# Kernel tuning notes

Hardware: AMD Instinct MI355X
Metric: run time of the kernel (lower is better)

## Reference

```python
import jax, jax.numpy as jnp
import numpy as np

B, TV, TE = 128, 32, 64
VOCAB, EMB, H, REPR, NET, MAXLEN = 1024, 256, 512, 128, 8, 32


def setup_inputs() -> dict:
    key = jax.random.key(0)
    ks = jax.random.split(key, 26)
    g = lambda i, shape: jax.random.normal(ks[i], shape, dtype=jnp.float32) * 0.05
    return dict(
        input_vertex=jax.random.randint(ks[0], (B, TV), 0, VOCAB),
        input_edge=jax.random.randint(ks[1], (B, TE, 3), 0, NET),
        vertex_emb=g(2, (VOCAB, EMB)),
        v_Wi=g(3, (3 * H, EMB)), v_Wh=g(4, (3 * H, H)), v_bi=g(5, (3 * H,)), v_bh=g(6, (3 * H,)),
        vout_W=g(7, (VOCAB, H)), vout_b=g(8, (VOCAB,)),
        vrep_W=g(9, (REPR, H)), vrep_b=g(10, (REPR,)),
        edge_emb=g(11, (MAXLEN, EMB)),
        e_Wi=g(12, (3 * H, 2 * EMB)), e_Wh=g(13, (3 * H, H)), e_bi=g(14, (3 * H,)), e_bh=g(15, (3 * H,)),
        erep_W=g(16, (REPR, H)), erep_b=g(17, (REPR,)),
        etype_W=g(18, (NET, REPR)), etype_b=g(19, (NET,)),
        src_w=g(20, (REPR,)), src_b=g(21, ()),
        dst_w=g(22, (REPR,)), dst_b=g(23, ()),
    )


def _gru_scan(X, Wi, Wh, bi, bh):
    # X: [T, B, D] -> hidden states [T, B, H]; torch GRUCell gate order r,z,n
    gi = jnp.einsum('tbd,gd->tbg', X, Wi) + bi  # precompute input projections
    h0 = jnp.zeros((X.shape[1], Wh.shape[1]), X.dtype)

    def step(h, gi_t):
        gh = h @ Wh.T + bh
        ir, iz, inn = jnp.split(gi_t, 3, axis=-1)
        hr, hz, hn = jnp.split(gh, 3, axis=-1)
        r = jax.nn.sigmoid(ir + hr)
        z = jax.nn.sigmoid(iz + hz)
        n = jnp.tanh(inn + r * hn)
        h_new = (1.0 - z) * n + z * h
        return h_new, h_new

    _, hs = jax.lax.scan(step, h0, gi)
    return hs


def reference(input_vertex, input_edge, vertex_emb, v_Wi, v_Wh, v_bi, v_bh,
              vout_W, vout_b, vrep_W, vrep_b, edge_emb, e_Wi, e_Wh, e_bi, e_bh,
              erep_W, erep_b, etype_W, etype_b, src_w, src_b, dst_w, dst_b):
    # ---- vertex RNN ----
    Ve = vertex_emb[input_vertex].transpose(1, 0, 2)          # [Tv, B, emb]
    hv = _gru_scan(Ve, v_Wi, v_Wh, v_bi, v_bh)                # [Tv, B, H]
    O_vertex = jnp.einsum('tbh,vh->bvt', hv, vout_W) + vout_b[None, :, None]  # [B, vocab, Tv]
    vrep = jnp.einsum('tbh,rh->tbr', hv, vrep_W) + vrep_b     # [Tv, B, repr]

    # ---- edge RNN ----
    E = jnp.concatenate([edge_emb[input_edge[:, :, 0]],
                         edge_emb[input_edge[:, :, 1]]], axis=2)  # [B, Te, 2*emb]
    he = _gru_scan(E.transpose(1, 0, 2), e_Wi, e_Wh, e_bi, e_bh)  # [Te, B, H]
    e = jnp.einsum('tbh,rh->tbr', he, erep_W) + erep_b            # [Te, B, repr]
    O_edge_type = jnp.einsum('ebr,kr->bke', e, etype_W) + etype_b[None, :, None]  # [B, n_et, Te]

    # ---- edge-vertex additive attention: tanh(e + v) ----
    u = jnp.tanh(e[:, None] + vrep[None])                     # [Te, Tv, B, repr]
    osrc = jnp.einsum('evbr,r->bve', u, src_w) + src_b        # [B, Tv, Te]
    odst = jnp.einsum('evbr,r->bve', u, dst_w) + dst_b        # [B, Tv, Te]
    O_edge = jnp.stack([osrc, odst], axis=2)                  # [B, Tv, 2, Te]

    return O_vertex, O_edge, O_edge_type
```

## Files before the change

### kernel.cpp

```cpp
#include <hip/hip_runtime.h>
#include <hip/hip_bf16.h>


typedef __bf16 bf16_t;
typedef bf16_t bf16x8 __attribute__((ext_vector_type(8)));
typedef bf16_t bf16x4 __attribute__((ext_vector_type(4)));
typedef float  f32x4  __attribute__((ext_vector_type(4)));

#define OFF_GIV  0ull
#define OFF_GIE  6291456ull
#define OFF_HV   18874368ull
#define OFF_HE   20971520ull
#define OFF_VREP 25165824ull
#define OFF_EREP 25690112ull
#define OFF_HBUF 26738688ull
#define FLAG_BYTE_OFF 54001664ull
#define OFF_CVT  27002880ull
#define CVT_VEMB  0ull
#define CVT_EEMB  262144ull
#define CVT_VWI   270336ull
#define CVT_EWI   663552ull
#define CVT_VWH   1449984ull
#define CVT_EWH   2236416ull
#define CVT_VOUT  3022848ull
#define CVT_VREPW 3547136ull
#define CVT_EREPW 3612672ull

#define OUT_OV 0ull
#define OUT_OE 4194304ull
#define OUT_OT 4718592ull

__device__ __forceinline__ float fsigmoid(float x) {
    float e = __builtin_amdgcn_exp2f(-x * 1.4426950408889634f);
    return __builtin_amdgcn_rcpf(1.0f + e);
}
__device__ __forceinline__ float ftanh(float x) {
    x = fminf(x, 15.0f);
    float e = __builtin_amdgcn_exp2f(x * 2.8853900817779268f);
    return (e - 1.0f) * __builtin_amdgcn_rcpf(e + 1.0f);
}

__global__ __launch_bounds__(256) void prep_kernel(
    const float* __restrict__ vemb, const float* __restrict__ eemb,
    const float* __restrict__ vwi,  const float* __restrict__ ewi,
    const float* __restrict__ vwh,  const float* __restrict__ ewh,
    const float* __restrict__ voutw, const float* __restrict__ vrepw,
    const float* __restrict__ erepw, bf16_t* __restrict__ cvt)
{
    int blk = blockIdx.x;
    const float* src; bf16_t* dst; int lb;
    if (blk < 256)       { src = vemb;  dst = cvt + CVT_VEMB;  lb = blk; }
    else if (blk < 264)  { src = eemb;  dst = cvt + CVT_EEMB;  lb = blk - 256; }
    else if (blk < 648)  { src = vwi;   dst = cvt + CVT_VWI;   lb = blk - 264; }
    else if (blk < 1416) { src = ewi;   dst = cvt + CVT_EWI;   lb = blk - 648; }
    else if (blk < 2184) { src = vwh;   dst = cvt + CVT_VWH;   lb = blk - 1416; }
    else if (blk < 2952) { src = ewh;   dst = cvt + CVT_EWH;   lb = blk - 2184; }
    else if (blk < 3464) { src = voutw; dst = cvt + CVT_VOUT;  lb = blk - 2952; }
    else if (blk < 3528) { src = vrepw; dst = cvt + CVT_VREPW; lb = blk - 3464; }
    else                 { src = erepw; dst = cvt + CVT_EREPW; lb = blk - 3528; }
    int idx = lb * 1024 + threadIdx.x * 4;
    float4 v = *(const float4*)(src + idx);
    bf16x4 o;
    o[0] = (bf16_t)v.x; o[1] = (bf16_t)v.y; o[2] = (bf16_t)v.z; o[3] = (bf16_t)v.w;
    *(bf16x4*)(dst + idx) = o;
}

template<int GATHER, int K>
__device__ __forceinline__ void produce_gi(
    const bf16_t* __restrict__ W, const float* __restrict__ bias,
    bf16_t* __restrict__ C, const int* __restrict__ gidx,
    const bf16_t* __restrict__ emb, int bx, int nbase)
{
    constexpr int K32 = K / 32;
    const int tid = threadIdx.x, lane = tid & 63, wv = tid >> 6;
    const int r16 = lane & 15, quad = lane >> 4, koff = quad * 8;
    const int mbase = bx * 512 + wv * 64;

    const bf16_t* ap0[4];
    const bf16_t* ap1[4];
#pragma unroll
    for (int i = 0; i < 4; ++i) {
        int row = mbase + i * 16 + r16;
        int b = row & 127, t = row >> 7;
        if (GATHER == 1) {
            ap0[i] = emb + (size_t)gidx[b * 32 + t] * 256 + koff;
            ap1[i] = ap0[i];
        } else {
            int c = (b * 64 + t) * 3;
            ap0[i] = emb + (size_t)gidx[c] * 256 + koff;
            ap1[i] = emb + (size_t)gidx[c + 1] * 256 + koff;
        }
    }
    const bf16_t* bp[4];
#pragma unroll
    for (int j = 0; j < 4; ++j)
        bp[j] = W + (size_t)(nbase + j * 16 + r16) * K + koff;

    f32x4 acc[4][4];
#pragma unroll
    for (int i = 0; i < 4; ++i)
#pragma unroll
        for (int j = 0; j < 4; ++j) acc[i][j] = (f32x4){0.f, 0.f, 0.f, 0.f};

    for (int kc = 0; kc < K32; ++kc) {
        bf16x8 a[4], b[4];
#pragma unroll
        for (int i = 0; i < 4; ++i) {
            const bf16_t* p;
            if (GATHER == 2) p = (kc < 8) ? (ap0[i] + kc * 32) : (ap1[i] + (kc - 8) * 32);
            else             p = ap0[i] + kc * 32;
            a[i] = *(const bf16x8*)p;
        }
#pragma unroll
        for (int j = 0; j < 4; ++j) b[j] = *(const bf16x8*)(bp[j] + kc * 32);
#pragma unroll
        for (int i = 0; i < 4; ++i)
#pragma unroll
            for (int j = 0; j < 4; ++j)
                acc[i][j] = __builtin_amdgcn_mfma_f32_16x16x32_bf16(a[i], b[j], acc[i][j], 0, 0, 0);
    }

#pragma unroll
    for (int j = 0; j < 4; ++j) {
        int col = nbase + j * 16 + r16;
        float bf = bias[col];
#pragma unroll
        for (int i = 0; i < 4; ++i) {
#pragma unroll
            for (int q = 0; q < 4; ++q) {
                int row = mbase + i * 16 + quad * 4 + q;
                C[(size_t)row * 1536 + col] = (bf16_t)(acc[i][j][q] + bf);
            }
        }
    }
}

__global__ __launch_bounds__(512) void produce_kernel(
    bf16_t* __restrict__ giV, bf16_t* __restrict__ giE,
    const int* __restrict__ ivtx, const int* __restrict__ iedg,
    const bf16_t* __restrict__ vemb, const bf16_t* __restrict__ eemb,
    const bf16_t* __restrict__ vwi, const bf16_t* __restrict__ ewi,
    const float* __restrict__ vbi, const float* __restrict__ ebi)
{
    int bid = blockIdx.x;
    if (bid < 192) {
        produce_gi<1, 256>(vwi, vbi, giV, ivtx, vemb, bid & 7, (bid >> 3) * 64);
    } else {
        int g3 = bid - 192;
        produce_gi<2, 512>(ewi, ebi, giE, iedg, eemb, g3 & 15, (g3 >> 4) * 64);
    }
}

__global__ __launch_bounds__(512)
__attribute__((amdgpu_waves_per_eu(2, 2)))
void gru_scan(
    const bf16_t* __restrict__ giV, const bf16_t* __restrict__ giE,
    const bf16_t* __restrict__ WhV, const bf16_t* __restrict__ WhE,
    const float* __restrict__ bhV, const float* __restrict__ bhE,
    bf16_t* __restrict__ hV, bf16_t* __restrict__ hE,
    bf16_t* __restrict__ hbuf, int* __restrict__ flags)
{
    __shared__ __align__(16) bf16_t hbf[2][16][520];
    __shared__ __align__(16) f32x4 red[4][3][64];
    const int bid = blockIdx.x;

    const int role = bid >> 6;
    const int lb   = bid & 63;
    const int g    = lb & 7;
    const int s    = lb >> 3;
    const bf16_t* gi = role ? giE : giV;
    const bf16_t* Wh = role ? WhE : WhV;
    const float*  bh = role ? bhE : bhV;
    bf16_t* hout = role ? hE : hV;
    const int T = role ? 64 : 32;
    const int slot = role * 8 + g;
    bf16_t* buf0 = hbuf + (size_t)slot * 2 * 8192;
    int* fl = flags + slot * 8;
    const int bb = g * 16;

    const int tid = threadIdx.x, lane = tid & 63, wv = tid >> 6;
    const int team = wv >> 1, half = wv & 1;
    const int r16 = lane & 15, quad = lane >> 4, koff = quad * 8;
    const int j = s * 64 + team * 16 + r16;
    const int kbase = half * 256;

    bf16x8 wfrag[3][8];
#pragma unroll
    for (int gate = 0; gate < 3; ++gate) {
        const bf16_t* wrow = Wh + ((size_t)(gate * 512 + j)) * 512 + kbase + koff;
#pragma unroll
        for (int kc = 0; kc < 8; ++kc)
            wfrag[gate][kc] = *(const bf16x8*)(wrow + kc * 32);
    }
    const float bhr = bh[j], bhz = bh[512 + j], bhn = bh[1024 + j];
    float hq[4] = {0.f, 0.f, 0.f, 0.f};

    for (int i = tid; i < 16 * 512; i += 512)
        hbf[0][i >> 9][i & 511] = (bf16_t)0.f;

    for (int t = 0; t < T; ++t) {
        if (t > 0) {
            if (wv == 1) {
                while (!__all((int)(__hip_atomic_load(&fl[lane & 7], __ATOMIC_RELAXED,
                                                      __HIP_MEMORY_SCOPE_AGENT) >= t))) { }
            }
            __syncthreads();
            asm volatile("" ::: "memory");
            unsigned long long* src = (unsigned long long*)(buf0 + (size_t)(t & 1) * 8192);
#pragma unroll
            for (int k = 0; k < 4; ++k) {
                int u = tid + k * 512;
                unsigned long long vv = __hip_atomic_load(src + u, __ATOMIC_RELAXED,
                                                          __HIP_MEMORY_SCOPE_AGENT);
                *(unsigned long long*)&hbf[t & 1][u >> 7][(u & 127) * 4] = vv;
            }
        }
        __syncthreads();

        float gv[3][4];
        if (half == 0) {
#pragma unroll
            for (int gg = 0; gg < 3; ++gg)
#pragma unroll
                for (int q = 0; q < 4; ++q)
                    gv[gg][q] = (float)gi[((size_t)(t * 128 + bb + quad * 4 + q)) * 1536
                                          + gg * 512 + j];
        }

        const bf16_t (*cur)[520] = hbf[t & 1];
        f32x4 ar = {0.f,0.f,0.f,0.f}, az = {0.f,0.f,0.f,0.f}, an = {0.f,0.f,0.f,0.f};
#pragma unroll
        for (int kc = 0; kc < 8; ++kc) {
            bf16x8 a = *(const bf16x8*)&cur[r16][kbase + kc * 32 + koff];
            ar = __builtin_amdgcn_mfma_f32_16x16x32_bf16(a, wfrag[0][kc], ar, 0, 0, 0);
            az = __builtin_amdgcn_mfma_f32_16x16x32_bf16(a, wfrag[1][kc], az, 0, 0, 0);
            an = __builtin_amdgcn_mfma_f32_16x16x32_bf16(a, wfrag[2][kc], an, 0, 0, 0);
        }

        if (half == 1) {
            red[team][0][lane] = ar;
            red[team][1][lane] = az;
            red[team][2][lane] = an;
        }
        __syncthreads();

        bf16_t hb4[4];
        if (half == 0) {
            ar += red[team][0][lane];
            az += red[team][1][lane];
            an += red[team][2][lane];
#pragma unroll
            for (int q = 0; q < 4; ++q) {
                float r = fsigmoid(gv[0][q] + ar[q] + bhr);
                float z = fsigmoid(gv[1][q] + az[q] + bhz);
                float n = ftanh(gv[2][q] + r * (an[q] + bhn));
                float hnew = (1.0f - z) * n + z * hq[q];
                hq[q] = hnew;
                hb4[q] = (bf16_t)hnew;
            }
            if (t + 1 < T) {
                bf16_t* dstg = buf0 + (size_t)((t + 1) & 1) * 8192;
#pragma unroll
                for (int q = 0; q < 4; ++q)
                    __hip_atomic_store((unsigned short*)(dstg + (quad * 4 + q) * 512 + j),
                                       __builtin_bit_cast(unsigned short, hb4[q]),
                                       __ATOMIC_RELAXED, __HIP_MEMORY_SCOPE_AGENT);
            }
        }

        if (t + 1 < T) {
            __builtin_amdgcn_s_waitcnt(0);
            __syncthreads();
            if (tid == 0)
                __hip_atomic_store(&fl[s], t + 1,
                                   __ATOMIC_RELAXED, __HIP_MEMORY_SCOPE_AGENT);
        } else {
            __syncthreads();
        }
        if (half == 0) {
#pragma unroll
            for (int q = 0; q < 4; ++q)
                hout[((size_t)((bb + quad * 4 + q) * T + t)) * 512 + j] = hb4[q];
        }
    }
}

template<int OUTMODE, int K>
__device__ __forceinline__ void consume_gemm(
    const bf16_t* __restrict__ A, const bf16_t* __restrict__ W,
    const float* __restrict__ bias, void* __restrict__ Cv,
    int N, int bx, int nbase)
{
    constexpr int K32 = K / 32;
    const int tid = threadIdx.x, lane = tid & 63, wv = tid >> 6;
    const int r16 = lane & 15, quad = lane >> 4, koff = quad * 8;
    const int mbase = bx * 512 + wv * 64;

    const bf16_t* ap[4];
#pragma unroll
    for (int i = 0; i < 4; ++i)
        ap[i] = A + (size_t)(mbase + i * 16 + r16) * K + koff;
    const bf16_t* bp[4];
#pragma unroll
    for (int j = 0; j < 4; ++j)
        bp[j] = W + (size_t)(nbase + j * 16 + r16) * K + koff;

    f32x4 acc[4][4];
#pragma unroll
    for (int i = 0; i < 4; ++i)
#pragma unroll
        for (int j = 0; j < 4; ++j) acc[i][j] = (f32x4){0.f, 0.f, 0.f, 0.f};

    for (int kc = 0; kc < K32; ++kc) {
        bf16x8 a[4], b[4];
#pragma unroll
        for (int i = 0; i < 4; ++i) a[i] = *(const bf16x8*)(ap[i] + kc * 32);
#pragma unroll
        for (int j = 0; j < 4; ++j) b[j] = *(const bf16x8*)(bp[j] + kc * 32);
#pragma unroll
        for (int i = 0; i < 4; ++i)
#pragma unroll
            for (int j = 0; j < 4; ++j)
                acc[i][j] = __builtin_amdgcn_mfma_f32_16x16x32_bf16(a[i], b[j], acc[i][j], 0, 0, 0);
    }

#pragma unroll
    for (int j = 0; j < 4; ++j) {
        int col = nbase + j * 16 + r16;
        float bf = bias[col];
#pragma unroll
        for (int i = 0; i < 4; ++i) {
            int rowq = mbase + i * 16 + quad * 4;
            if (OUTMODE == 1) {
                int b = rowq >> 5, t0 = rowq & 31;
                float4 v4;
                v4.x = acc[i][j][0] + bf; v4.y = acc[i][j][1] + bf;
                v4.z = acc[i][j][2] + bf; v4.w = acc[i][j][3] + bf;
                *(float4*)((float*)Cv + ((size_t)(b * 1024) + col) * 32 + t0) = v4;
            } else {
                bf16_t* C = (bf16_t*)Cv;
#pragma unroll
                for (int q = 0; q < 4; ++q)
                    C[(size_t)(rowq + q) * N + col] = (bf16_t)(acc[i][j][q] + bf);
            }
        }
    }
}

__global__ __launch_bounds__(512) void consume_kernel(
    const bf16_t* __restrict__ hV, const bf16_t* __restrict__ hE,
    const bf16_t* __restrict__ voutw, const float* __restrict__ voutb,
    const bf16_t* __restrict__ vrepw, const float* __restrict__ vrepb,
    const bf16_t* __restrict__ erepw, const float* __restrict__ erepb,
    bf16_t* __restrict__ vrep, bf16_t* __restrict__ erep,
    float* __restrict__ out)
{
    int bid = blockIdx.x;
    if (bid < 128) {
        consume_gemm<1, 512>(hV, voutw, voutb, out, 1024, bid & 7, (bid >> 3) * 64);
    } else if (bid < 144) {
        int cb = bid - 128;
        consume_gemm<0, 512>(hV, vrepw, vrepb, vrep, 128, cb & 7, (cb >> 3) * 64);
    } else {
        int cb = bid - 144;
        consume_gemm<0, 512>(hE, erepw, erepb, erep, 128, cb & 15, (cb >> 4) * 64);
    }
}

__global__ __launch_bounds__(256) void etype_kernel(
    const bf16_t* __restrict__ erep, const float* __restrict__ W,
    const float* __restrict__ bias, float* __restrict__ out)
{
    int o = blockIdx.x * 256 + threadIdx.x;
    int te = o & 63, k = (o >> 6) & 7, b = o >> 9;
    float sacc = bias[k];
    const bf16_t* e = erep + ((size_t)(b * 64 + te)) * 128;
    const float* w = W + k * 128;
#pragma unroll 8
    for (int r = 0; r < 128; ++r) sacc += (float)e[r] * w[r];
    out[OUT_OT + o] = sacc;
}

__global__ __launch_bounds__(256) void attn_kernel(
    const bf16_t* __restrict__ erep, const bf16_t* __restrict__ vrep,
    const float* __restrict__ src_w, const float* __restrict__ src_b,
    const float* __restrict__ dst_w, const float* __restrict__ dst_b,
    float* __restrict__ out)
{
    int b = blockIdx.x >> 1, half = blockIdx.x & 1;
    __shared__ float es[32][129], vs[32][129], swf[128], dwf[128];
    int tid = threadIdx.x;
    for (int f = tid; f < 32 * 128; f += 256) {
        int i = f >> 7, r = f & 127;
        es[i][r] = (float)erep[((size_t)(b * 64 + half * 32 + i)) * 128 + r];
        vs[i][r] = (float)vrep[((size_t)(b * 32 + i)) * 128 + r];
    }
    if (tid < 128) { swf[tid] = src_w[tid]; dwf[tid] = dst_w[tid]; }
    __syncthreads();
    float sb = src_b[0], db = dst_b[0];
    for (int p = tid; p < 1024; p += 256) {
        int te = p & 31, tv = p >> 5;
        float sacc = 0.f, dacc = 0.f;
#pragma unroll 4
        for (int r = 0; r < 128; ++r) {
            float u = ftanh(es[te][r] + vs[tv][r]);
            sacc += u * swf[r];
            dacc += u * dwf[r];
        }
        int teg = half * 32 + te;
        size_t base = OUT_OE + ((size_t)(b * 32 + tv) * 2) * 64;
        out[base + teg]      = sacc + sb;
        out[base + 64 + teg] = dacc + db;
    }
}

extern "C" void kernel_launch(void* const* d_in, const int* in_sizes, int n_in,
                              void* d_out, int out_size, void* d_ws, size_t ws_size,
                              hipStream_t stream)
{
    const int*   input_vertex = (const int*)d_in[0];
    const int*   input_edge   = (const int*)d_in[1];
    const float* vertex_emb   = (const float*)d_in[2];
    const float* v_Wi  = (const float*)d_in[3];
    const float* v_Wh  = (const float*)d_in[4];
    const float* v_bi  = (const float*)d_in[5];
    const float* v_bh  = (const float*)d_in[6];
    const float* vout_W = (const float*)d_in[7];
    const float* vout_b = (const float*)d_in[8];
    const float* vrep_W = (const float*)d_in[9];
    const float* vrep_b = (const float*)d_in[10];
    const float* edge_emb = (const float*)d_in[11];
    const float* e_Wi  = (const float*)d_in[12];
    const float* e_Wh  = (const float*)d_in[13];
    const float* e_bi  = (const float*)d_in[14];
    const float* e_bh  = (const float*)d_in[15];
    const float* erep_W = (const float*)d_in[16];
    const float* erep_b = (const float*)d_in[17];
    const float* etype_W = (const float*)d_in[18];
    const float* etype_b = (const float*)d_in[19];
    const float* src_w = (const float*)d_in[20];
    const float* src_b = (const float*)d_in[21];
    const float* dst_w = (const float*)d_in[22];
    const float* dst_b = (const float*)d_in[23];

    bf16_t* ws   = (bf16_t*)d_ws;
    bf16_t* giV  = ws + OFF_GIV;
    bf16_t* giE  = ws + OFF_GIE;
    bf16_t* hV   = ws + OFF_HV;
    bf16_t* hE   = ws + OFF_HE;
    bf16_t* vrep = ws + OFF_VREP;
    bf16_t* erep = ws + OFF_EREP;
    bf16_t* hbuf = ws + OFF_HBUF;
    bf16_t* cvt  = ws + OFF_CVT;
    int*    flags = (int*)((char*)d_ws + FLAG_BYTE_OFF);
    float*  out  = (float*)d_out;

    prep_kernel<<<3592, 256, 0, stream>>>(vertex_emb, edge_emb, v_Wi, e_Wi, v_Wh, e_Wh,
                                          vout_W, vrep_W, erep_W, cvt);

    produce_kernel<<<576, 512, 0, stream>>>(giV, giE, input_vertex, input_edge,
                                            cvt + CVT_VEMB, cvt + CVT_EEMB,
                                            cvt + CVT_VWI, cvt + CVT_EWI, v_bi, e_bi);

    gru_scan<<<128, 512, 0, stream>>>(giV, giE, cvt + CVT_VWH, cvt + CVT_EWH,
                                      v_bh, e_bh, hV, hE, hbuf, flags);

    consume_kernel<<<176, 512, 0, stream>>>(hV, hE, cvt + CVT_VOUT, vout_b,
                                            cvt + CVT_VREPW, vrep_b,
                                            cvt + CVT_EREPW, erep_b, vrep, erep, out);

    etype_kernel<<<256, 256, 0, stream>>>(erep, etype_W, etype_b, out);
    attn_kernel<<<256, 256, 0, stream>>>(erep, vrep, src_w, src_b, dst_w, dst_b, out);
}
```

Measured before the change: 480.5 us.

## Fuse fp32-to-bf16 conversion into GEMMs and repartition GRU scan across blocks

Removes the separate weight/embedding conversion kernel and converts fp32 to bf16 on load inside the GEMM and GRU kernels. The GRU scan is repartitioned: each 128-thread block now handles 32 hidden columns for 32 batch rows with Wh cached in LDS instead of registers, dropping the intra-block K-split reduction. The gi loads are hoisted ahead of the flag wait. The etype and attention kernels are merged into one launch. This cuts launches and a global round trip, but the producer and consumer GEMMs now re-read fp32 data and convert it on every load. The scan spreads 16 flags per slot and copies more shared state per step.

```diff
diff --git a/kernel.cpp b/kernel.cpp
--- a/kernel.cpp
+++ b/kernel.cpp
@@ -6,6 +6,7 @@
 typedef bf16_t bf16x8 __attribute__((ext_vector_type(8)));
 typedef bf16_t bf16x4 __attribute__((ext_vector_type(4)));
 typedef float  f32x4  __attribute__((ext_vector_type(4)));
+typedef unsigned long long ull_t;
 
 #define OFF_GIV  0ull
 #define OFF_GIE  6291456ull
@@ -15,16 +16,6 @@
 #define OFF_EREP 25690112ull
 #define OFF_HBUF 26738688ull
 #define FLAG_BYTE_OFF 54001664ull
-#define OFF_CVT  27002880ull
-#define CVT_VEMB  0ull
-#define CVT_EEMB  262144ull
-#define CVT_VWI   270336ull
-#define CVT_EWI   663552ull
-#define CVT_VWH   1449984ull
-#define CVT_EWH   2236416ull
-#define CVT_VOUT  3022848ull
-#define CVT_VREPW 3547136ull
-#define CVT_EREPW 3612672ull
 
 #define OUT_OV 0ull
 #define OUT_OE 4194304ull
@@ -39,45 +30,28 @@
     float e = __builtin_amdgcn_exp2f(x * 2.8853900817779268f);
     return (e - 1.0f) * __builtin_amdgcn_rcpf(e + 1.0f);
 }
-
-__global__ __launch_bounds__(256) void prep_kernel(
-    const float* __restrict__ vemb, const float* __restrict__ eemb,
-    const float* __restrict__ vwi,  const float* __restrict__ ewi,
-    const float* __restrict__ vwh,  const float* __restrict__ ewh,
-    const float* __restrict__ voutw, const float* __restrict__ vrepw,
-    const float* __restrict__ erepw, bf16_t* __restrict__ cvt)
-{
-    int blk = blockIdx.x;
-    const float* src; bf16_t* dst; int lb;
-    if (blk < 256)       { src = vemb;  dst = cvt + CVT_VEMB;  lb = blk; }
-    else if (blk < 264)  { src = eemb;  dst = cvt + CVT_EEMB;  lb = blk - 256; }
-    else if (blk < 648)  { src = vwi;   dst = cvt + CVT_VWI;   lb = blk - 264; }
-    else if (blk < 1416) { src = ewi;   dst = cvt + CVT_EWI;   lb = blk - 648; }
-    else if (blk < 2184) { src = vwh;   dst = cvt + CVT_VWH;   lb = blk - 1416; }
-    else if (blk < 2952) { src = ewh;   dst = cvt + CVT_EWH;   lb = blk - 2184; }
-    else if (blk < 3464) { src = voutw; dst = cvt + CVT_VOUT;  lb = blk - 2952; }
-    else if (blk < 3528) { src = vrepw; dst = cvt + CVT_VREPW; lb = blk - 3464; }
-    else                 { src = erepw; dst = cvt + CVT_EREPW; lb = blk - 3528; }
-    int idx = lb * 1024 + threadIdx.x * 4;
-    float4 v = *(const float4*)(src + idx);
-    bf16x4 o;
-    o[0] = (bf16_t)v.x; o[1] = (bf16_t)v.y; o[2] = (bf16_t)v.z; o[3] = (bf16_t)v.w;
-    *(bf16x4*)(dst + idx) = o;
+__device__ __forceinline__ bf16x8 ld_cvt8(const float* p) {
+    float4 a = *(const float4*)p;
+    float4 b = *(const float4*)(p + 4);
+    bf16x8 r;
+    r[0] = (bf16_t)a.x; r[1] = (bf16_t)a.y; r[2] = (bf16_t)a.z; r[3] = (bf16_t)a.w;
+    r[4] = (bf16_t)b.x; r[5] = (bf16_t)b.y; r[6] = (bf16_t)b.z; r[7] = (bf16_t)b.w;
+    return r;
 }
 
 template<int GATHER, int K>
 __device__ __forceinline__ void produce_gi(
-    const bf16_t* __restrict__ W, const float* __restrict__ bias,
+    const float* __restrict__ W, const float* __restrict__ bias,
     bf16_t* __restrict__ C, const int* __restrict__ gidx,
-    const bf16_t* __restrict__ emb, int bx, int nbase)
+    const float* __restrict__ emb, int bx, int nbase)
 {
     constexpr int K32 = K / 32;
     const int tid = threadIdx.x, lane = tid & 63, wv = tid >> 6;
     const int r16 = lane & 15, quad = lane >> 4, koff = quad * 8;
     const int mbase = bx * 512 + wv * 64;
 
-    const bf16_t* ap0[4];
-    const bf16_t* ap1[4];
+    const float* ap0[4];
+    const float* ap1[4];
 #pragma unroll
     for (int i = 0; i < 4; ++i) {
         int row = mbase + i * 16 + r16;
@@ -91,7 +65,7 @@
             ap1[i] = emb + (size_t)gidx[c + 1] * 256 + koff;
         }
     }
-    const bf16_t* bp[4];
+    const float* bp[4];
 #pragma unroll
     for (int j = 0; j < 4; ++j)
         bp[j] = W + (size_t)(nbase + j * 16 + r16) * K + koff;
@@ -106,13 +80,13 @@
         bf16x8 a[4], b[4];
 #pragma unroll
         for (int i = 0; i < 4; ++i) {
-            const bf16_t* p;
+            const float* p;
             if (GATHER == 2) p = (kc < 8) ? (ap0[i] + kc * 32) : (ap1[i] + (kc - 8) * 32);
             else             p = ap0[i] + kc * 32;
-            a[i] = *(const bf16x8*)p;
-        }
-#pragma unroll
-        for (int j = 0; j < 4; ++j) b[j] = *(const bf16x8*)(bp[j] + kc * 32);
+            a[i] = ld_cvt8(p);
+        }
+#pragma unroll
+        for (int j = 0; j < 4; ++j) b[j] = ld_cvt8(bp[j] + kc * 32);
 #pragma unroll
         for (int i = 0; i < 4; ++i)
 #pragma unroll
@@ -138,8 +112,8 @@
 __global__ __launch_bounds__(512) void produce_kernel(
     bf16_t* __restrict__ giV, bf16_t* __restrict__ giE,
     const int* __restrict__ ivtx, const int* __restrict__ iedg,
-    const bf16_t* __restrict__ vemb, const bf16_t* __restrict__ eemb,
-    const bf16_t* __restrict__ vwi, const bf16_t* __restrict__ ewi,
+    const float* __restrict__ vemb, const float* __restrict__ eemb,
+    const float* __restrict__ vwi, const float* __restrict__ ewi,
     const float* __restrict__ vbi, const float* __restrict__ ebi)
 {
     int bid = blockIdx.x;
@@ -151,143 +125,138 @@
     }
 }
 
-__global__ __launch_bounds__(512)
-__attribute__((amdgpu_waves_per_eu(2, 2)))
-void gru_scan(
+__global__ __launch_bounds__(128) void gru_scan(
     const bf16_t* __restrict__ giV, const bf16_t* __restrict__ giE,
-    const bf16_t* __restrict__ WhV, const bf16_t* __restrict__ WhE,
+    const float* __restrict__ WhVf, const float* __restrict__ WhEf,
     const float* __restrict__ bhV, const float* __restrict__ bhE,
     bf16_t* __restrict__ hV, bf16_t* __restrict__ hE,
     bf16_t* __restrict__ hbuf, int* __restrict__ flags)
 {
-    __shared__ __align__(16) bf16_t hbf[2][16][520];
-    __shared__ __align__(16) f32x4 red[4][3][64];
-    const int bid = blockIdx.x;
-
-    const int role = bid >> 6;
-    const int lb   = bid & 63;
-    const int g    = lb & 7;
-    const int s    = lb >> 3;
-    const bf16_t* gi = role ? giE : giV;
-    const bf16_t* Wh = role ? WhE : WhV;
-    const float*  bh = role ? bhE : bhV;
+    __shared__ __align__(16) bf16_t WhL[3][32][520];
+    __shared__ __align__(16) bf16_t hbf[32][520];
+
+    const int bid  = blockIdx.x;
+    const int slot = bid & 7;
+    const int s    = bid >> 3;
+    const int role = slot >> 2;
+    const int g    = slot & 3;
+    const bf16_t* gi  = role ? giE : giV;
+    const float*  Whf = role ? WhEf : WhVf;
+    const float*  bh  = role ? bhE : bhV;
     bf16_t* hout = role ? hE : hV;
     const int T = role ? 64 : 32;
-    const int slot = role * 8 + g;
-    bf16_t* buf0 = hbuf + (size_t)slot * 2 * 8192;
-    int* fl = flags + slot * 8;
-    const int bb = g * 16;
-
-    const int tid = threadIdx.x, lane = tid & 63, wv = tid >> 6;
-    const int team = wv >> 1, half = wv & 1;
+    bf16_t* buf0 = hbuf + (size_t)slot * 32768;
+    int* fl = flags + slot * 16;
+    const int bb = g * 32;
+    const int colbase = s * 32;
+
+    const int tid = threadIdx.x, lane = tid & 63, w = tid >> 6;
     const int r16 = lane & 15, quad = lane >> 4, koff = quad * 8;
-    const int j = s * 64 + team * 16 + r16;
-    const int kbase = half * 256;
-
-    bf16x8 wfrag[3][8];
-#pragma unroll
-    for (int gate = 0; gate < 3; ++gate) {
-        const bf16_t* wrow = Wh + ((size_t)(gate * 512 + j)) * 512 + kbase + koff;
-#pragma unroll
-        for (int kc = 0; kc < 8; ++kc)
-            wfrag[gate][kc] = *(const bf16x8*)(wrow + kc * 32);
-    }
+    const int j = colbase + w * 16 + r16;
+
+    for (int u = tid; u < 3 * 32 * 128; u += 128) {
+        int gate = u >> 12, rr = u & 4095;
+        int c = rr >> 7, k4 = (rr & 127) << 2;
+        float4 v = *(const float4*)(Whf + ((size_t)(gate * 512 + colbase + c)) * 512 + k4);
+        bf16x4 o;
+        o[0] = (bf16_t)v.x; o[1] = (bf16_t)v.y; o[2] = (bf16_t)v.z; o[3] = (bf16_t)v.w;
+        *(bf16x4*)&WhL[gate][c][k4] = o;
+    }
+    for (int u = tid; u < 32 * 520; u += 128)
+        ((bf16_t*)hbf)[u] = (bf16_t)0.f;
     const float bhr = bh[j], bhz = bh[512 + j], bhn = bh[1024 + j];
-    float hq[4] = {0.f, 0.f, 0.f, 0.f};
-
-    for (int i = tid; i < 16 * 512; i += 512)
-        hbf[0][i >> 9][i & 511] = (bf16_t)0.f;
+    float hq[2][4] = {{0.f,0.f,0.f,0.f},{0.f,0.f,0.f,0.f}};
+    __syncthreads();
 
     for (int t = 0; t < T; ++t) {
+        float gv[3][2][4];
+#pragma unroll
+        for (int gg = 0; gg < 3; ++gg)
+#pragma unroll
+            for (int rt = 0; rt < 2; ++rt)
+#pragma unroll
+                for (int q = 0; q < 4; ++q)
+                    gv[gg][rt][q] = (float)gi[((size_t)(t * 128 + bb + rt * 16 + quad * 4 + q)) * 1536
+                                              + gg * 512 + j];
+
         if (t > 0) {
-            if (wv == 1) {
-                while (!__all((int)(__hip_atomic_load(&fl[lane & 7], __ATOMIC_RELAXED,
+            if (w == 0) {
+                while (!__all((int)(__hip_atomic_load(&fl[lane & 15], __ATOMIC_RELAXED,
                                                       __HIP_MEMORY_SCOPE_AGENT) >= t))) { }
             }
             __syncthreads();
             asm volatile("" ::: "memory");
-            unsigned long long* src = (unsigned long long*)(buf0 + (size_t)(t & 1) * 8192);
-#pragma unroll
-            for (int k = 0; k < 4; ++k) {
-                int u = tid + k * 512;
-                unsigned long long vv = __hip_atomic_load(src + u, __ATOMIC_RELAXED,
-                                                          __HIP_MEMORY_SCOPE_AGENT);
-                *(unsigned long long*)&hbf[t & 1][u >> 7][(u & 127) * 4] = vv;
+            ull_t* src = (ull_t*)(buf0 + (size_t)(t & 1) * 16384);
+#pragma unroll
+            for (int k = 0; k < 32; ++k) {
+                int u = tid + k * 128;
+                ull_t vv = __hip_atomic_load(src + u, __ATOMIC_RELAXED,
+                                             __HIP_MEMORY_SCOPE_AGENT);
+                *(ull_t*)&hbf[u >> 7][(u & 127) * 4] = vv;
             }
         }
         __syncthreads();
 
-        float gv[3][4];
-        if (half == 0) {
-#pragma unroll
-            for (int gg = 0; gg < 3; ++gg)
+        f32x4 acc[3][2];
+#pragma unroll
+        for (int gg = 0; gg < 3; ++gg)
+#pragma unroll
+            for (int rt = 0; rt < 2; ++rt) acc[gg][rt] = (f32x4){0.f, 0.f, 0.f, 0.f};
+#pragma unroll
+        for (int kc = 0; kc < 16; ++kc) {
+            bf16x8 a0 = *(const bf16x8*)&hbf[r16][kc * 32 + koff];
+            bf16x8 a1 = *(const bf16x8*)&hbf[16 + r16][kc * 32 + koff];
+            bf16x8 b0 = *(const bf16x8*)&WhL[0][w * 16 + r16][kc * 32 + koff];
+            bf16x8 b1 = *(const bf16x8*)&WhL[1][w * 16 + r16][kc * 32 + koff];
+            bf16x8 b2 = *(const bf16x8*)&WhL[2][w * 16 + r16][kc * 32 + koff];
+            acc[0][0] = __builtin_amdgcn_mfma_f32_16x16x32_bf16(a0, b0, acc[0][0], 0, 0, 0);
+            acc[0][1] = __builtin_amdgcn_mfma_f32_16x16x32_bf16(a1, b0, acc[0][1], 0, 0, 0);
+            acc[1][0] = __builtin_amdgcn_mfma_f32_16x16x32_bf16(a0, b1, acc[1][0], 0, 0, 0);
+            acc[1][1] = __builtin_amdgcn_mfma_f32_16x16x32_bf16(a1, b1, acc[1][1], 0, 0, 0);
+            acc[2][0] = __builtin_amdgcn_mfma_f32_16x16x32_bf16(a0, b2, acc[2][0], 0, 0, 0);
+            acc[2][1] = __builtin_amdgcn_mfma_f32_16x16x32_bf16(a1, b2, acc[2][1], 0, 0, 0);
+        }
+
+        bf16_t hb[2][4];
+#pragma unroll
+        for (int rt = 0; rt < 2; ++rt)
+#pragma unroll
+            for (int q = 0; q < 4; ++q) {
+                float r = fsigmoid(gv[0][rt][q] + acc[0][rt][q] + bhr);
+                float z = fsigmoid(gv[1][rt][q] + acc[1][rt][q] + bhz);
+                float n = ftanh(gv[2][rt][q] + r * (acc[2][rt][q] + bhn));
+                float hnew = (1.0f - z) * n + z * hq[rt][q];
+                hq[rt][q] = hnew;
+                hb[rt][q] = (bf16_t)hnew;
+            }
+
+        if (t + 1 < T) {
+            bf16_t* dstg = buf0 + (size_t)((t + 1) & 1) * 16384;
+#pragma unroll
+            for (int rt = 0; rt < 2; ++rt)
 #pragma unroll
                 for (int q = 0; q < 4; ++q)
-                    gv[gg][q] = (float)gi[((size_t)(t * 128 + bb + quad * 4 + q)) * 1536
-                                          + gg * 512 + j];
-        }
-
-        const bf16_t (*cur)[520] = hbf[t & 1];
-        f32x4 ar = {0.f,0.f,0.f,0.f}, az = {0.f,0.f,0.f,0.f}, an = {0.f,0.f,0.f,0.f};
-#pragma unroll
-        for (int kc = 0; kc < 8; ++kc) {
-            bf16x8 a = *(const bf16x8*)&cur[r16][kbase + kc * 32 + koff];
-            ar = __builtin_amdgcn_mfma_f32_16x16x32_bf16(a, wfrag[0][kc], ar, 0, 0, 0);
-            az = __builtin_amdgcn_mfma_f32_16x16x32_bf16(a, wfrag[1][kc], az, 0, 0, 0);
-            an = __builtin_amdgcn_mfma_f32_16x16x32_bf16(a, wfrag[2][kc], an, 0, 0, 0);
-        }
-
-        if (half == 1) {
-            red[team][0][lane] = ar;
-            red[team][1][lane] = az;
-            red[team][2][lane] = an;
-        }
-        __syncthreads();
-
-        bf16_t hb4[4];
-        if (half == 0) {
-            ar += red[team][0][lane];
-            az += red[team][1][lane];
-            an += red[team][2][lane];
-#pragma unroll
-            for (int q = 0; q < 4; ++q) {
-                float r = fsigmoid(gv[0][q] + ar[q] + bhr);
-                float z = fsigmoid(gv[1][q] + az[q] + bhz);
-                float n = ftanh(gv[2][q] + r * (an[q] + bhn));
-                float hnew = (1.0f - z) * n + z * hq[q];
-                hq[q] = hnew;
-                hb4[q] = (bf16_t)hnew;
-            }
-            if (t + 1 < T) {
-                bf16_t* dstg = buf0 + (size_t)((t + 1) & 1) * 8192;
-#pragma unroll
-                for (int q = 0; q < 4; ++q)
-                    __hip_atomic_store((unsigned short*)(dstg + (quad * 4 + q) * 512 + j),
-                                       __builtin_bit_cast(unsigned short, hb4[q]),
-                                       __ATOMIC_RELAXED, __HIP_MEMORY_SCOPE_AGENT);
-            }
-        }
-
-        if (t + 1 < T) {
+                    __hip_atomic_store(
+                        (unsigned short*)(dstg + (rt * 16 + quad * 4 + q) * 512 + j),
+                        __builtin_bit_cast(unsigned short, hb[rt][q]),
+                        __ATOMIC_RELAXED, __HIP_MEMORY_SCOPE_AGENT);
             __builtin_amdgcn_s_waitcnt(0);
             __syncthreads();
             if (tid == 0)
                 __hip_atomic_store(&fl[s], t + 1,
                                    __ATOMIC_RELAXED, __HIP_MEMORY_SCOPE_AGENT);
-        } else {
-            __syncthreads();
-        }
-        if (half == 0) {
+        }
+#pragma unroll
+        for (int rt = 0; rt < 2; ++rt)
 #pragma unroll
             for (int q = 0; q < 4; ++q)
-                hout[((size_t)((bb + quad * 4 + q) * T + t)) * 512 + j] = hb4[q];
-        }
+                hout[((size_t)((bb + rt * 16 + quad * 4 + q) * T + t)) * 512 + j] = hb[rt][q];
     }
 }
 
 template<int OUTMODE, int K>
 __device__ __forceinline__ void consume_gemm(
-    const bf16_t* __restrict__ A, const bf16_t* __restrict__ W,
+    const bf16_t* __restrict__ A, const float* __restrict__ W,
     const float* __restrict__ bias, void* __restrict__ Cv,
     int N, int bx, int nbase)
 {
@@ -300,7 +269,7 @@
 #pragma unroll
     for (int i = 0; i < 4; ++i)
         ap[i] = A + (size_t)(mbase + i * 16 + r16) * K + koff;
-    const bf16_t* bp[4];
+    const float* bp[4];
 #pragma unroll
     for (int j = 0; j < 4; ++j)
         bp[j] = W + (size_t)(nbase + j * 16 + r16) * K + koff;
@@ -316,7 +285,7 @@
 #pragma unroll
         for (int i = 0; i < 4; ++i) a[i] = *(const bf16x8*)(ap[i] + kc * 32);
 #pragma unroll
-        for (int j = 0; j < 4; ++j) b[j] = *(const bf16x8*)(bp[j] + kc * 32);
+        for (int j = 0; j < 4; ++j) b[j] = ld_cvt8(bp[j] + kc * 32);
 #pragma unroll
         for (int i = 0; i < 4; ++i)
 #pragma unroll
@@ -349,9 +318,9 @@
 
 __global__ __launch_bounds__(512) void consume_kernel(
     const bf16_t* __restrict__ hV, const bf16_t* __restrict__ hE,
-    const bf16_t* __restrict__ voutw, const float* __restrict__ voutb,
-    const bf16_t* __restrict__ vrepw, const float* __restrict__ vrepb,
-    const bf16_t* __restrict__ erepw, const float* __restrict__ erepb,
+    const float* __restrict__ voutw, const float* __restrict__ voutb,
+    const float* __restrict__ vrepw, const float* __restrict__ vrepb,
+    const float* __restrict__ erepw, const float* __restrict__ erepb,
     bf16_t* __restrict__ vrep, bf16_t* __restrict__ erep,
     float* __restrict__ out)
 {
@@ -367,29 +336,28 @@
     }
 }
 
-__global__ __launch_bounds__(256) void etype_kernel(
-    const bf16_t* __restrict__ erep, const float* __restrict__ W,
-    const float* __restrict__ bias, float* __restrict__ out)
-{
-    int o = blockIdx.x * 256 + threadIdx.x;
-    int te = o & 63, k = (o >> 6) & 7, b = o >> 9;
-    float sacc = bias[k];
-    const bf16_t* e = erep + ((size_t)(b * 64 + te)) * 128;
-    const float* w = W + k * 128;
-#pragma unroll 8
-    for (int r = 0; r < 128; ++r) sacc += (float)e[r] * w[r];
-    out[OUT_OT + o] = sacc;
-}
-
-__global__ __launch_bounds__(256) void attn_kernel(
+__global__ __launch_bounds__(256) void tail_kernel(
     const bf16_t* __restrict__ erep, const bf16_t* __restrict__ vrep,
+    const float* __restrict__ etypeW, const float* __restrict__ etypeB,
     const float* __restrict__ src_w, const float* __restrict__ src_b,
     const float* __restrict__ dst_w, const float* __restrict__ dst_b,
     float* __restrict__ out)
 {
-    int b = blockIdx.x >> 1, half = blockIdx.x & 1;
     __shared__ float es[32][129], vs[32][129], swf[128], dwf[128];
     int tid = threadIdx.x;
+    if (blockIdx.x < 256) {
+        int o = blockIdx.x * 256 + tid;
+        int te = o & 63, k = (o >> 6) & 7, b = o >> 9;
+        float sacc = etypeB[k];
+        const bf16_t* e = erep + ((size_t)(b * 64 + te)) * 128;
+        const float* w = etypeW + k * 128;
+#pragma unroll 8
+        for (int r = 0; r < 128; ++r) sacc += (float)e[r] * w[r];
+        out[OUT_OT + o] = sacc;
+        return;
+    }
+    int abid = blockIdx.x - 256;
+    int b = abid >> 1, half = abid & 1;
     for (int f = tid; f < 32 * 128; f += 256) {
         int i = f >> 7, r = f & 127;
         es[i][r] = (float)erep[((size_t)(b * 64 + half * 32 + i)) * 128 + r];
@@ -451,24 +419,20 @@
     bf16_t* vrep = ws + OFF_VREP;
     bf16_t* erep = ws + OFF_EREP;
     bf16_t* hbuf = ws + OFF_HBUF;
-    bf16_t* cvt  = ws + OFF_CVT;
     int*    flags = (int*)((char*)d_ws + FLAG_BYTE_OFF);
     float*  out  = (float*)d_out;
 
-    prep_kernel<<<3592, 256, 0, stream>>>(vertex_emb, edge_emb, v_Wi, e_Wi, v_Wh, e_Wh,
-                                          vout_W, vrep_W, erep_W, cvt);
-
     produce_kernel<<<576, 512, 0, stream>>>(giV, giE, input_vertex, input_edge,
-                                            cvt + CVT_VEMB, cvt + CVT_EEMB,
-                                            cvt + CVT_VWI, cvt + CVT_EWI, v_bi, e_bi);
-
-    gru_scan<<<128, 512, 0, stream>>>(giV, giE, cvt + CVT_VWH, cvt + CVT_EWH,
-                                      v_bh, e_bh, hV, hE, hbuf, flags);
-
-    consume_kernel<<<176, 512, 0, stream>>>(hV, hE, cvt + CVT_VOUT, vout_b,
-                                            cvt + CVT_VREPW, vrep_b,
-                                            cvt + CVT_EREPW, erep_b, vrep, erep, out);
-
-    etype_kernel<<<256, 256, 0, stream>>>(erep, etype_W, etype_b, out);
-    attn_kernel<<<256, 256, 0, stream>>>(erep, vrep, src_w, src_b, dst_w, dst_b, out);
-}
+                                            vertex_emb, edge_emb, v_Wi, e_Wi,
+                                            v_bi, e_bi);
+
+    gru_scan<<<128, 128, 0, stream>>>(giV, giE, v_Wh, e_Wh, v_bh, e_bh,
+                                      hV, hE, hbuf, flags);
+
+    consume_kernel<<<176, 512, 0, stream>>>(hV, hE, vout_W, vout_b,
+                                            vrep_W, vrep_b, erep_W, erep_b,
+                                            vrep, erep, out);
+
+    tail_kernel<<<512, 256, 0, stream>>>(erep, vrep, etype_W, etype_b,
+                                         src_w, src_b, dst_w, dst_b, out);
+}
```

Result: slower. 1.000 ms (+108.2%).

## Repartition GRU scan to 32-row batch groups with LDS-resident recurrent weights

Applied to the files above, without the earlier changes.

Reworks the cross-block split of the GRU recurrence. Each block now owns 32 hidden columns for 32 batch rows, with 16 column-slice blocks per group, instead of 64 columns for 16 rows. The recurrent weight slice is staged in shared memory rather than held in registers, the waves-per-EU attribute is dropped, and the gi loads are hoisted ahead of the flag wait. The aim is to cut the number of batch groups and per-step flag traffic and to lower register pressure. In exchange, B operands are re-read from LDS every step and each block waits on more peers and copies twice the hidden state per step.

```diff
diff --git a/kernel.cpp b/kernel.cpp
--- a/kernel.cpp
+++ b/kernel.cpp
@@ -6,6 +6,7 @@
 typedef bf16_t bf16x8 __attribute__((ext_vector_type(8)));
 typedef bf16_t bf16x4 __attribute__((ext_vector_type(4)));
 typedef float  f32x4  __attribute__((ext_vector_type(4)));
+typedef unsigned long long ull_t;
 
 #define OFF_GIV  0ull
 #define OFF_GIE  6291456ull
@@ -151,90 +152,93 @@
     }
 }
 
-__global__ __launch_bounds__(512)
-__attribute__((amdgpu_waves_per_eu(2, 2)))
-void gru_scan(
+__global__ __launch_bounds__(512) void gru_scan(
     const bf16_t* __restrict__ giV, const bf16_t* __restrict__ giE,
     const bf16_t* __restrict__ WhV, const bf16_t* __restrict__ WhE,
     const float* __restrict__ bhV, const float* __restrict__ bhE,
     bf16_t* __restrict__ hV, bf16_t* __restrict__ hE,
     bf16_t* __restrict__ hbuf, int* __restrict__ flags)
 {
-    __shared__ __align__(16) bf16_t hbf[2][16][520];
+    __shared__ __align__(16) bf16_t WhL[3][32][520];
+    __shared__ __align__(16) bf16_t hbf[32][520];
     __shared__ __align__(16) f32x4 red[4][3][64];
-    const int bid = blockIdx.x;
-
-    const int role = bid >> 6;
-    const int lb   = bid & 63;
-    const int g    = lb & 7;
-    const int s    = lb >> 3;
+
+    const int bid  = blockIdx.x;
+    const int slot = bid & 7;
+    const int s    = bid >> 3;
+    const int role = slot >> 2;
+    const int g    = slot & 3;
     const bf16_t* gi = role ? giE : giV;
     const bf16_t* Wh = role ? WhE : WhV;
     const float*  bh = role ? bhE : bhV;
     bf16_t* hout = role ? hE : hV;
     const int T = role ? 64 : 32;
-    const int slot = role * 8 + g;
-    bf16_t* buf0 = hbuf + (size_t)slot * 2 * 8192;
-    int* fl = flags + slot * 8;
-    const int bb = g * 16;
-
-    const int tid = threadIdx.x, lane = tid & 63, wv = tid >> 6;
-    const int team = wv >> 1, half = wv & 1;
+    bf16_t* buf0 = hbuf + (size_t)slot * 32768;
+    int* fl = flags + slot * 16;
+    const int bb = g * 32;
+    const int colbase = s * 32;
+
+    const int tid = threadIdx.x, lane = tid & 63, w = tid >> 6;
+    const int team = w >> 1, half = w & 1;
+    const int cs = team >> 1, rt = team & 1;
     const int r16 = lane & 15, quad = lane >> 4, koff = quad * 8;
-    const int j = s * 64 + team * 16 + r16;
+    const int cj = cs * 16 + r16;
+    const int j = colbase + cj;
     const int kbase = half * 256;
 
-    bf16x8 wfrag[3][8];
-#pragma unroll
-    for (int gate = 0; gate < 3; ++gate) {
-        const bf16_t* wrow = Wh + ((size_t)(gate * 512 + j)) * 512 + kbase + koff;
-#pragma unroll
-        for (int kc = 0; kc < 8; ++kc)
-            wfrag[gate][kc] = *(const bf16x8*)(wrow + kc * 32);
-    }
+    for (int u = tid; u < 6144; u += 512) {
+        int gate = u >> 11;
+        int rr = u & 2047;
+        int c = rr >> 6, k8 = rr & 63;
+        bf16x8 v = *(const bf16x8*)(Wh + ((size_t)(gate * 512 + colbase + c)) * 512 + k8 * 8);
+        *(bf16x8*)&WhL[gate][c][k8 * 8] = v;
+    }
+    for (int u = tid; u < 32 * 520; u += 512)
+        ((bf16_t*)hbf)[u] = (bf16_t)0.f;
     const float bhr = bh[j], bhz = bh[512 + j], bhn = bh[1024 + j];
     float hq[4] = {0.f, 0.f, 0.f, 0.f};
-
-    for (int i = tid; i < 16 * 512; i += 512)
-        hbf[0][i >> 9][i & 511] = (bf16_t)0.f;
+    __syncthreads();
 
     for (int t = 0; t < T; ++t) {
+        float gv[3][4];
+        if (half == 0) {
+#pragma unroll
+            for (int gg = 0; gg < 3; ++gg)
+#pragma unroll
+                for (int q = 0; q < 4; ++q)
+                    gv[gg][q] = (float)gi[((size_t)(t * 128 + bb + rt * 16 + quad * 4 + q)) * 1536
+                                          + gg * 512 + j];
+        }
+
         if (t > 0) {
-            if (wv == 1) {
-                while (!__all((int)(__hip_atomic_load(&fl[lane & 7], __ATOMIC_RELAXED,
+            if (w == 1) {
+                while (!__all((int)(__hip_atomic_load(&fl[lane & 15], __ATOMIC_RELAXED,
                                                       __HIP_MEMORY_SCOPE_AGENT) >= t))) { }
             }
             __syncthreads();
             asm volatile("" ::: "memory");
-            unsigned long long* src = (unsigned long long*)(buf0 + (size_t)(t & 1) * 8192);
-#pragma unroll
-            for (int k = 0; k < 4; ++k) {
+            ull_t* src = (ull_t*)(buf0 + (size_t)(t & 1) * 16384);
+#pragma unroll
+            for (int k = 0; k < 8; ++k) {
                 int u = tid + k * 512;
-                unsigned long long vv = __hip_atomic_load(src + u, __ATOMIC_RELAXED,
-                                                          __HIP_MEMORY_SCOPE_AGENT);
-                *(unsigned long long*)&hbf[t & 1][u >> 7][(u & 127) * 4] = vv;
+                ull_t vv = __hip_atomic_load(src + u, __ATOMIC_RELAXED,
+                                             __HIP_MEMORY_SCOPE_AGENT);
+                *(ull_t*)&hbf[u >> 7][(u & 127) * 4] = vv;
             }
         }
         __syncthreads();
 
-        float gv[3][4];
-        if (half == 0) {
-#pragma unroll
-            for (int gg = 0; gg < 3; ++gg)
-#pragma unroll
-                for (int q = 0; q < 4; ++q)
-                    gv[gg][q] = (float)gi[((size_t)(t * 128 + bb + quad * 4 + q)) * 1536
-                                          + gg * 512 + j];
-        }
-
-        const bf16_t (*cur)[520] = hbf[t & 1];
         f32x4 ar = {0.f,0.f,0.f,0.f}, az = {0.f,0.f,0.f,0.f}, an = {0.f,0.f,0.f,0.f};
 #pragma unroll
         for (int kc = 0; kc < 8; ++kc) {
-            bf16x8 a = *(const bf16x8*)&cur[r16][kbase + kc * 32 + koff];
-            ar = __builtin_amdgcn_mfma_f32_16x16x32_bf16(a, wfrag[0][kc], ar, 0, 0, 0);
-            az = __builtin_amdgcn_mfma_f32_16x16x32_bf16(a, wfrag[1][kc], az, 0, 0, 0);
-            an = __builtin_amdgcn_mfma_f32_16x16x32_bf16(a, wfrag[2][kc], an, 0, 0, 0);
+            int ko = kbase + kc * 32 + koff;
+            bf16x8 a  = *(const bf16x8*)&hbf[rt * 16 + r16][ko];
+            bf16x8 b0 = *(const bf16x8*)&WhL[0][cj][ko];
+            bf16x8 b1 = *(const bf16x8*)&WhL[1][cj][ko];
+            bf16x8 b2 = *(const bf16x8*)&WhL[2][cj][ko];
+            ar = __builtin_amdgcn_mfma_f32_16x16x32_bf16(a, b0, ar, 0, 0, 0);
+            az = __builtin_amdgcn_mfma_f32_16x16x32_bf16(a, b1, az, 0, 0, 0);
+            an = __builtin_amdgcn_mfma_f32_16x16x32_bf16(a, b2, an, 0, 0, 0);
         }
 
         if (half == 1) {
@@ -259,12 +263,13 @@
                 hb4[q] = (bf16_t)hnew;
             }
             if (t + 1 < T) {
-                bf16_t* dstg = buf0 + (size_t)((t + 1) & 1) * 8192;
+                bf16_t* dstg = buf0 + (size_t)((t + 1) & 1) * 16384;
 #pragma unroll
                 for (int q = 0; q < 4; ++q)
-                    __hip_atomic_store((unsigned short*)(dstg + (quad * 4 + q) * 512 + j),
-                                       __builtin_bit_cast(unsigned short, hb4[q]),
-                                       __ATOMIC_RELAXED, __HIP_MEMORY_SCOPE_AGENT);
+                    __hip_atomic_store(
+                        (unsigned short*)(dstg + (rt * 16 + quad * 4 + q) * 512 + j),
+                        __builtin_bit_cast(unsigned short, hb4[q]),
+                        __ATOMIC_RELAXED, __HIP_MEMORY_SCOPE_AGENT);
             }
         }
 
@@ -280,7 +285,7 @@
         if (half == 0) {
 #pragma unroll
             for (int q = 0; q < 4; ++q)
-                hout[((size_t)((bb + quad * 4 + q) * T + t)) * 512 + j] = hb4[q];
+                hout[((size_t)((bb + rt * 16 + quad * 4 + q) * T + t)) * 512 + j] = hb4[q];
         }
     }
 }
```

Result: slower. 571.2 us (+18.9%).
